# Kernel optimization log

Measured on AMD Instinct MI355X. Metric: run time of the kernel, lower is better.

## Reference

```python
import jax, jax.numpy as jnp
import numpy as np

B, N, C, H = 2, 1024, 1024, 16
HD = C // H
PAST = 8192
CACHE_BUDGET = 4000
ANCHOR = 512            # anchor_token_count (first-frame tokens preserved)
IMP_W = 0.5             # importance_weight
SCALE = HD ** -0.5


def setup_inputs() -> dict:
    key = jax.random.key(0)
    ks = jax.random.split(key, 8)
    return {
        "x": jax.random.normal(ks[0], (B, N, C), jnp.float32),
        "past_k": jax.random.normal(ks[1], (B, H, PAST, HD), jnp.float32),
        "past_v": jax.random.normal(ks[2], (B, H, PAST, HD), jnp.float32),
        "importance_scores": jax.random.uniform(ks[3], (B, N), dtype=jnp.float32),
        "qkv_w": jax.random.normal(ks[4], (3 * C, C), jnp.float32) * 0.02,
        "qkv_b": jnp.zeros((3 * C,), jnp.float32),
        "proj_w": jax.random.normal(ks[5], (C, C), jnp.float32) * 0.02,
        "proj_b": jnp.zeros((C,), jnp.float32),
    }


def _eviction(k, v, imp):
    # k, v: [B, H, Ntot, D]; imp: [B, N_new]. Hybrid branch of Attention.eviction.
    Bb, Hh, Ntot, D = k.shape
    A = ANCHOR
    Nc = Ntot - A                      # candidates
    keep = CACHE_BUDGET - A            # num_to_keep_from_candidates
    n_old = Nc - N                     # old (past-frame) candidates
    anchor_k, cand_k = k[:, :, :A], k[:, :, A:]
    anchor_v, cand_v = v[:, :, :A], v[:, :, A:]
    # cosine-diversity baseline (F.normalize uses eps=1e-12)
    kn = cand_k / jnp.maximum(jnp.linalg.norm(cand_k, axis=-1, keepdims=True), 1e-12)
    mean_vec = kn.mean(axis=2, keepdims=True)              # [B,H,1,D]
    baseline = jnp.sum(kn * mean_vec, axis=-1)             # [B,H,Nc]
    div_avg = (1.0 - baseline).mean(axis=1)                # [B,Nc]
    old = div_avg[:, :n_old]
    old_n = (old - old.min(axis=-1, keepdims=True)) / (
        old.max(axis=-1, keepdims=True) - old.min(axis=-1, keepdims=True) + 1e-8)
    new_n = (imp - imp.min(axis=-1, keepdims=True)) / (
        imp.max(axis=-1, keepdims=True) - imp.min(axis=-1, keepdims=True) + 1e-8)
    combined = jnp.concatenate([(1.0 - IMP_W) * old_n, IMP_W * new_n], axis=-1)  # [B,Nc]
    _, idx = jax.lax.top_k(combined, keep)
    idx = jnp.sort(idx, axis=-1)                           # [B,keep]
    gidx = jnp.broadcast_to(idx[:, None, :, None], (Bb, Hh, keep, D))
    kept_k = jnp.take_along_axis(cand_k, gidx, axis=2)
    kept_v = jnp.take_along_axis(cand_v, gidx, axis=2)
    return (jnp.concatenate([anchor_k, kept_k], axis=2),
            jnp.concatenate([anchor_v, kept_v], axis=2))


def reference(x, past_k, past_v, importance_scores, qkv_w, qkv_b, proj_w, proj_b):
    # qkv projection -> [3, B, H, N, HD]
    qkv = (x @ qkv_w.T + qkv_b).reshape(B, N, 3, H, HD).transpose(2, 0, 3, 1, 4)
    q, k, v = qkv[0], qkv[1], qkv[2]
    # append to KV cache
    k = jnp.concatenate([past_k, k], axis=2)
    v = jnp.concatenate([past_v, v], axis=2)
    # KV-cache eviction (topk importance + cosine diversity + gather compaction)
    k, v = _eviction(k, v, importance_scores)              # [B,H,CACHE_BUDGET,HD]
    # scaled dot-product attention
    attn = jax.nn.softmax(jnp.einsum('bhqd,bhkd->bhqk', q, k) * SCALE, axis=-1)
    out = jnp.einsum('bhqk,bhkd->bhqd', attn, v)
    out = out.transpose(0, 2, 1, 3).reshape(B, N, C)
    return out @ proj_w.T + proj_b
```

## Files before the change

kernel.cpp:

```cpp
#include <hip/hip_runtime.h>
#include <hip/hip_bf16.h>

typedef unsigned short u16;
typedef unsigned int   u32;
typedef __attribute__((ext_vector_type(8)))  short v8s;
typedef __attribute__((ext_vector_type(4)))  float v4f;
typedef __attribute__((ext_vector_type(16))) float v16f;
typedef __attribute__((ext_vector_type(4)))  u32   v4u;
typedef __attribute__((ext_vector_type(2)))  u32   v2u;

#define B_      2
#define N_      1024
#define C_      1024
#define H_      16
#define BH_     32
#define PAST_   8192
#define BUDGET  4000
#define ANCHOR_ 512
#define NCAND   8704
#define NOLD    7680
#define KEEPN   3488
#define NSPLIT  4
#define QSCALE  0.18033688011112042f

__device__ __forceinline__ u16 f2bf(float f) {
    u32 u = __float_as_uint(f);
    u32 r = u + 0x7fffu + ((u >> 16) & 1u);
    return (u16)(r >> 16);
}
__device__ __forceinline__ float bf2f(u16 h) {
    return __uint_as_float(((u32)h) << 16);
}
__device__ __forceinline__ u32 pk2(float a, float b) {
    __hip_bfloat162 t = __float22bfloat162_rn(float2{a, b});
    u32 r; __builtin_memcpy(&r, &t, 4); return r;
}
__device__ __forceinline__ v8s mk8(u32 a, u32 b, u32 c, u32 d) {
    union { u32 u[4]; v8s s; } t; t.u[0]=a; t.u[1]=b; t.u[2]=c; t.u[3]=d; return t.s;
}

__global__ void prep(const float* __restrict__ x, const float* __restrict__ qw,
                     const float* __restrict__ pw, u16* __restrict__ xcat,
                     u16* __restrict__ wcat, u16* __restrict__ wpbf) {
    const int i = blockIdx.x * 256 + threadIdx.x;
    const int NX = 2048 * 1024, NW = 3072 * 1024;
    if (i < NX) {
        float v = x[i];
        u16 hi = f2bf(v); float lo = v - bf2f(hi);
        const int m = i >> 10, k = i & 1023;
        u16* p = xcat + (size_t)m * 3072 + k;
        p[0] = hi; p[1024] = hi; p[2048] = f2bf(lo);
    } else if (i < NX + NW) {
        const int j = i - NX;
        float v = qw[j];
        u16 hi = f2bf(v); float lo = v - bf2f(hi);
        const int n = j >> 10, k = j & 1023;
        u16* p = wcat + (size_t)n * 3072 + k;
        p[0] = hi; p[1024] = f2bf(lo); p[2048] = hi;
    } else {
        const int j = i - NX - NW;
        wpbf[j] = f2bf(pw[j]);
    }
}

__global__ __launch_bounds__(256) void gemm_qkv(
    const u16* __restrict__ A, const u16* __restrict__ Bm,
    const float* __restrict__ bias,
    u16* __restrict__ Qbf, float* __restrict__ Vnew, float* __restrict__ Kpart) {
    __shared__ u16 As[128 * 72];
    __shared__ u16 Bs[128 * 72];
    const int tid = threadIdx.x;
    const int l = tid & 63, w = tid >> 6;
    const int wm = w >> 1, wn = w & 1;
    const int bid = blockIdx.x;
    int tsel, by, bx, s;
    if (bid < 128)      { tsel = 0; by = bid >> 3; bx = bid & 7; s = 0; }
    else if (bid < 256) { int r = bid - 128; tsel = 2; by = r >> 3; bx = r & 7; s = 0; }
    else                { int r = bid - 256; s = r >> 7; r &= 127; tsel = 1; by = r >> 3; bx = r & 7; }
    const int ks = s * 1024;
    const int nbase = tsel * 1024 + bx * 128;

    v4f acc[4][4];
    #pragma unroll
    for (int a = 0; a < 4; ++a)
        #pragma unroll
        for (int b = 0; b < 4; ++b) { acc[a][b][0]=0.f; acc[a][b][1]=0.f; acc[a][b][2]=0.f; acc[a][b][3]=0.f; }

    const int srow = tid >> 1, shalf = tid & 1;
    const u16* pa = A  + ((size_t)(by * 128 + srow)) * 3072 + ks + shalf * 32;
    const u16* pb = Bm + ((size_t)(nbase + srow))    * 3072 + ks + shalf * 32;
    v4u ar[4], br[4];
    #pragma unroll
    for (int j = 0; j < 4; ++j) { ar[j] = *(const v4u*)(pa + j * 8); br[j] = *(const v4u*)(pb + j * 8); }

    for (int k0 = 0; k0 < 1024; k0 += 64) {
        #pragma unroll
        for (int j = 0; j < 4; ++j) {
            *(v4u*)(&As[srow * 72 + shalf * 32 + j * 8]) = ar[j];
            *(v4u*)(&Bs[srow * 72 + shalf * 32 + j * 8]) = br[j];
        }
        __syncthreads();
        if (k0 + 64 < 1024) {
            #pragma unroll
            for (int j = 0; j < 4; ++j) {
                ar[j] = *(const v4u*)(pa + (k0 + 64) + j * 8);
                br[j] = *(const v4u*)(pb + (k0 + 64) + j * 8);
            }
        }
        #pragma unroll
        for (int kc = 0; kc < 2; ++kc) {
            v8s af[4], bfr[4];
            #pragma unroll
            for (int mt = 0; mt < 4; ++mt)
                af[mt] = *(const v8s*)(&As[(wm * 64 + mt * 16 + (l & 15)) * 72 + kc * 32 + (l >> 4) * 8]);
            #pragma unroll
            for (int nt = 0; nt < 4; ++nt)
                bfr[nt] = *(const v8s*)(&Bs[(wn * 64 + nt * 16 + (l & 15)) * 72 + kc * 32 + (l >> 4) * 8]);
            #pragma unroll
            for (int mt = 0; mt < 4; ++mt)
                #pragma unroll
                for (int nt = 0; nt < 4; ++nt)
                    acc[mt][nt] = __builtin_amdgcn_mfma_f32_16x16x32_bf16(af[mt], bfr[nt], acc[mt][nt], 0, 0, 0);
        }
        __syncthreads();
    }
    #pragma unroll
    for (int nt = 0; nt < 4; ++nt) {
        const int nl = bx * 128 + wn * 64 + nt * 16 + (l & 15);
        const int hh = nl >> 6, dd = nl & 63;
        const float bv = bias[tsel * 1024 + nl];
        #pragma unroll
        for (int mt = 0; mt < 4; ++mt)
            #pragma unroll
            for (int r = 0; r < 4; ++r) {
                const int m = by * 128 + wm * 64 + mt * 16 + (l >> 4) * 4 + r;
                const int bb = m >> 10, nn = m & 1023;
                const size_t o = (((size_t)(bb * 16 + hh)) * 1024 + nn) * 64 + dd;
                if (tsel == 0)      Qbf[o] = f2bf((acc[mt][nt][r] + bv) * QSCALE);
                else if (tsel == 2) Vnew[o] = acc[mt][nt][r] + bv;
                else                Kpart[(size_t)s * 2097152 + o] = acc[mt][nt][r] + (s == 0 ? bv : 0.f);
            }
    }
}

__global__ void kred(float* __restrict__ Kp) {
    const size_t i = ((size_t)blockIdx.x * 256 + threadIdx.x) * 4;
    v4f a = *(const v4f*)(Kp + i);
    v4f b = *(const v4f*)(Kp + 2097152 + i);
    v4f c = *(const v4f*)(Kp + 4194304 + i);
    #pragma unroll
    for (int e = 0; e < 4; ++e) a[e] = (a[e] + b[e]) + c[e];
    *(v4f*)(Kp + i) = a;
}

__global__ __launch_bounds__(256) void kmean(const float* __restrict__ past_k,
                                             const float* __restrict__ Knew,
                                             float* __restrict__ part) {
    __shared__ float Asum[4][64];
    const int blk = blockIdx.x, tid = threadIdx.x;
    const int bh = blk / 34, seg = blk % 34;
    const int l = tid & 63, w = tid >> 6;
    const int rr = l >> 4, dd = l & 15;
    v4f acc; acc[0]=0.f; acc[1]=0.f; acc[2]=0.f; acc[3]=0.f;
    const int base = seg * 256 + w * 64;
    for (int q4 = 0; q4 < 64; q4 += 4) {
        const int i = base + q4 + rr;
        const float* rp = (i < NOLD)
            ? past_k + (((size_t)bh * PAST_) + ANCHOR_ + i) * 64
            : Knew   + (((size_t)bh * N_) + (i - NOLD)) * 64;
        v4f v = *(const v4f*)(rp + dd * 4);
        float ss = v[0]*v[0] + v[1]*v[1] + v[2]*v[2] + v[3]*v[3];
        ss += __shfl_xor(ss, 1); ss += __shfl_xor(ss, 2);
        ss += __shfl_xor(ss, 4); ss += __shfl_xor(ss, 8);
        const float rn = 1.0f / fmaxf(sqrtf(ss), 1e-12f);
        acc[0] += v[0]*rn; acc[1] += v[1]*rn; acc[2] += v[2]*rn; acc[3] += v[3]*rn;
    }
    #pragma unroll
    for (int e = 0; e < 4; ++e) { acc[e] += __shfl_xor(acc[e], 16); acc[e] += __shfl_xor(acc[e], 32); }
    if (l < 16) *(v4f*)(&Asum[w][dd * 4]) = acc;
    __syncthreads();
    if (tid < 64) {
        float s = Asum[0][tid] + Asum[1][tid] + Asum[2][tid] + Asum[3][tid];
        part[((size_t)seg * BH_ + bh) * 64 + tid] = s;
    }
}

__global__ void kmr(const float* __restrict__ part, float* __restrict__ msum) {
    const int i = blockIdx.x * 256 + threadIdx.x;
    if (i < 2048) {
        float s = 0.f;
        for (int g = 0; g < 34; ++g) s += part[(size_t)g * 2048 + i];
        msum[i] = s;
    }
}

__global__ __launch_bounds__(256) void kdiv(const float* __restrict__ past_k,
                                            const float* __restrict__ msum,
                                            float* __restrict__ divavg) {
    __shared__ float MV[1024];
    const int blk = blockIdx.x, tid = threadIdx.x;
    const int b = blk / 240, ib = blk % 240;
    for (int j = tid; j < 1024; j += 256) MV[j] = msum[(size_t)b * 1024 + j] / 8704.0f;
    __syncthreads();
    const int l = tid & 63, w = tid >> 6;
    const int rr = l >> 4, dd = l & 15;
    for (int ii = 0; ii < 8; ++ii) {
        const int i = ib * 32 + w * 8 + ii;
        float accv = 0.f;
        #pragma unroll
        for (int hq = 0; hq < 4; ++hq) {
            const int h = hq * 4 + rr;
            const v4f v  = *(const v4f*)(past_k + (((size_t)(b * 16 + h)) * PAST_ + ANCHOR_ + i) * 64 + dd * 4);
            const v4f mv = *(const v4f*)(&MV[h * 64 + dd * 4]);
            float ss = v[0]*v[0] + v[1]*v[1] + v[2]*v[2] + v[3]*v[3];
            float dp = v[0]*mv[0] + v[1]*mv[1] + v[2]*mv[2] + v[3]*mv[3];
            ss += __shfl_xor(ss, 1); dp += __shfl_xor(dp, 1);
            ss += __shfl_xor(ss, 2); dp += __shfl_xor(dp, 2);
            ss += __shfl_xor(ss, 4); dp += __shfl_xor(dp, 4);
            ss += __shfl_xor(ss, 8); dp += __shfl_xor(dp, 8);
            accv += 1.0f - dp / fmaxf(sqrtf(ss), 1e-12f);
        }
        accv += __shfl_xor(accv, 16); accv += __shfl_xor(accv, 32);
        if (l == 0) divavg[(size_t)b * NOLD + i] = accv / 16.0f;
    }
}

__global__ __launch_bounds__(256) void kselect(const float* __restrict__ divavg,
                                               const float* __restrict__ imp,
                                               int* __restrict__ keep) {
    __shared__ float comb[NCAND];
    __shared__ float red[16];
    __shared__ u32 scnt[2][4];
    __shared__ u32 sg[257], se[257];
    const int b = blockIdx.x, tid = threadIdx.x;
    const int l = tid & 63, w = tid >> 6;

    float mn = 1e30f, mx = -1e30f;
    for (int i = tid; i < NOLD; i += 256) { float v = divavg[b * NOLD + i]; mn = fminf(mn, v); mx = fmaxf(mx, v); }
    #pragma unroll
    for (int d = 1; d < 64; d <<= 1) { mn = fminf(mn, __shfl_xor(mn, d)); mx = fmaxf(mx, __shfl_xor(mx, d)); }
    if (l == 0) { red[w] = mn; red[4 + w] = mx; }
    float mn2 = 1e30f, mx2 = -1e30f;
    for (int i = tid; i < N_; i += 256) { float v = imp[b * N_ + i]; mn2 = fminf(mn2, v); mx2 = fmaxf(mx2, v); }
    #pragma unroll
    for (int d = 1; d < 64; d <<= 1) { mn2 = fminf(mn2, __shfl_xor(mn2, d)); mx2 = fmaxf(mx2, __shfl_xor(mx2, d)); }
    if (l == 0) { red[8 + w] = mn2; red[12 + w] = mx2; }
    __syncthreads();
    const float omin = fminf(fminf(red[0], red[1]), fminf(red[2], red[3]));
    const float omax = fmaxf(fmaxf(red[4], red[5]), fmaxf(red[6], red[7]));
    const float imin = fminf(fminf(red[8], red[9]), fminf(red[10], red[11]));
    const float imax = fmaxf(fmaxf(red[12], red[13]), fmaxf(red[14], red[15]));
    const float oden = omax - omin + 1e-8f, iden = imax - imin + 1e-8f;
    for (int i = tid; i < NCAND; i += 256)
        comb[i] = (i < NOLD) ? 0.5f * ((divavg[b * NOLD + i] - omin) / oden)
                             : 0.5f * ((imp[b * N_ + i - NOLD] - imin) / iden);
    __syncthreads();
    u32 fu[34];
    const int i0 = tid * 34;
    #pragma unroll
    for (int j = 0; j < 34; ++j) fu[j] = __float_as_uint(comb[i0 + j]);
    u32 lo = 0, hi = 0x3F000000u;
    int it = 0;
    while (lo < hi) {
        const u32 mid = lo + ((hi - lo) >> 1);
        u32 c = 0;
        #pragma unroll
        for (int j = 0; j < 34; ++j) c += (fu[j] > mid) ? 1u : 0u;
        c += __shfl_xor(c, 1); c += __shfl_xor(c, 2); c += __shfl_xor(c, 4);
        c += __shfl_xor(c, 8); c += __shfl_xor(c, 16); c += __shfl_xor(c, 32);
        if (l == 0) scnt[it & 1][w] = c;
        __syncthreads();
        const u32 total = scnt[it & 1][0] + scnt[it & 1][1] + scnt[it & 1][2] + scnt[it & 1][3];
        if (total < KEEPN) hi = mid; else lo = mid + 1;
        ++it;
    }
    const u32 tau = lo;
    u32 ng = 0, ne = 0;
    #pragma unroll
    for (int j = 0; j < 34; ++j) { ng += (fu[j] > tau); ne += (fu[j] == tau); }
    sg[tid + 1] = ng; se[tid + 1] = ne;
    __syncthreads();
    if (tid == 0) { sg[0] = 0; se[0] = 0; for (int t = 1; t <= 256; ++t) { sg[t] += sg[t - 1]; se[t] += se[t - 1]; } }
    __syncthreads();
    const u32 need = KEEPN - sg[256];
    u32 g = sg[tid], e = se[tid];
    #pragma unroll
    for (int j = 0; j < 34; ++j) {
        const u32 u = fu[j];
        const bool kg = u > tau;
        const bool ke = (u == tau) && (e < need);
        if (kg || ke) keep[b * KEEPN + (g + (e < need ? e : need))] = 512 + i0 + j;
        g += kg ? 1u : 0u; e += (u == tau) ? 1u : 0u;
    }
}

__global__ __launch_bounds__(256) void kgather(const float* __restrict__ past_k,
    const float* __restrict__ past_v, const float* __restrict__ Knew,
    const float* __restrict__ Vnew, const int* __restrict__ keep,
    u16* __restrict__ Kg, u16* __restrict__ VTg) {
    __shared__ float VL[64][65];
    const int blk = blockIdx.x, tid = threadIdx.x;
    const int bh = blk / 63, jb = blk % 63;
    const int b = bh >> 4;
    const int jj = tid >> 2, cc = tid & 3;
    const int j = jb * 64 + jj;
    if (j < BUDGET) {
        const int row = (j < ANCHOR_) ? j : keep[b * KEEPN + (j - ANCHOR_)];
        const float *ks, *vs;
        if (row < PAST_) { size_t o = ((size_t)bh * PAST_ + row) * 64; ks = past_k + o; vs = past_v + o; }
        else             { size_t o = ((size_t)bh * N_ + (row - PAST_)) * 64; ks = Knew + o; vs = Vnew + o; }
        union { u16 h[16]; v4u v[2]; } pk_;
        #pragma unroll
        for (int q4 = 0; q4 < 4; ++q4) {
            v4f kv = *(const v4f*)(ks + cc * 16 + q4 * 4);
            v4f vv = *(const v4f*)(vs + cc * 16 + q4 * 4);
            #pragma unroll
            for (int e = 0; e < 4; ++e) {
                pk_.h[q4 * 4 + e] = f2bf(kv[e]);
                VL[jj][cc * 16 + q4 * 4 + e] = vv[e];
            }
        }
        v4u* kout = (v4u*)(Kg + ((size_t)bh * BUDGET + j) * 64 + cc * 16);
        kout[0] = pk_.v[0]; kout[1] = pk_.v[1];
    }
    __syncthreads();
    const int d = tid >> 2, c4 = tid & 3;
    const int jc = c4 * 16;
    if (jb * 64 + jc < BUDGET) {
        union { u16 h[16]; v4u v[2]; } pv_;
        #pragma unroll
        for (int t2 = 0; t2 < 16; ++t2) pv_.h[t2] = f2bf(VL[jc + t2][d]);
        v4u* vout = (v4u*)(VTg + ((size_t)bh * 64 + d) * BUDGET + jb * 64 + jc);
        vout[0] = pv_.v[0]; vout[1] = pv_.v[1];
    }
}

__global__ __launch_bounds__(256) void attn(const u16* __restrict__ Qbf,
    const u16* __restrict__ Kg, const u16* __restrict__ VTg,
    float* __restrict__ Opart, float* __restrict__ Mpart, float* __restrict__ Lpart) {
    __shared__ u16 Ks[2][32 * 72];
    __shared__ u16 Vs[2][64 * 40];
    const int tid = threadIdx.x;
    const int l = tid & 63, w = tid >> 6;
    const int G = l >> 5, lq = l & 31;
    const int bid = blockIdx.x;
    const int bh = bid >> 5, rem = bid & 31;
    const int split = rem & 3, qblk = rem >> 2;
    const int q = qblk * 128 + w * 32 + lq;
    const int t0 = split * 32;
    const int t1 = (split == 3) ? 125 : (t0 + 32);

    v8s Qf[4];
    const v8s* qp = (const v8s*)(Qbf + ((size_t)(bh * 1024 + q)) * 64);
    #pragma unroll
    for (int c = 0; c < 4; ++c) Qf[c] = qp[c * 2 + G];

    v16f o0, o1;
    #pragma unroll
    for (int e = 0; e < 16; ++e) { o0[e] = 0.f; o1[e] = 0.f; }
    float mrun = -1e30f, lrun = 0.f;

    const int krow = tid >> 3, kc8 = tid & 7;
    const int vrow = tid >> 2, vc4 = tid & 3;
    const u16* kbase = Kg + ((size_t)bh * BUDGET + krow) * 64 + kc8 * 8;
    const u16* vbase = VTg + ((size_t)bh * 64 + vrow) * BUDGET + vc4 * 8;
    v4u kreg = *(const v4u*)(kbase + (size_t)t0 * 2048);
    v4u vreg = *(const v4u*)(vbase + t0 * 32);
    int cur = 0;

    for (int t = t0; t < t1; ++t) {
        *(v4u*)(&Ks[cur][krow * 72 + kc8 * 8]) = kreg;
        *(v4u*)(&Vs[cur][vrow * 40 + vc4 * 8]) = vreg;
        if (t + 1 < t1) {
            kreg = *(const v4u*)(kbase + (size_t)(t + 1) * 2048);
            vreg = *(const v4u*)(vbase + (t + 1) * 32);
        }
        __syncthreads();
        v16f s;
        #pragma unroll
        for (int e = 0; e < 16; ++e) s[e] = 0.f;
        v8s kf[4];
        #pragma unroll
        for (int c = 0; c < 4; ++c) kf[c] = *(const v8s*)(&Ks[cur][lq * 72 + c * 16 + G * 8]);
        #pragma unroll
        for (int c = 0; c < 4; ++c)
            s = __builtin_amdgcn_mfma_f32_32x32x16_bf16(kf[c], Qf[c], s, 0, 0, 0);
        float m0 = fmaxf(s[0], s[1]),  m1 = fmaxf(s[2], s[3]),  m2 = fmaxf(s[4], s[5]),  m3 = fmaxf(s[6], s[7]);
        float m4 = fmaxf(s[8], s[9]),  m5 = fmaxf(s[10], s[11]), m6 = fmaxf(s[12], s[13]), m7 = fmaxf(s[14], s[15]);
        float mt = fmaxf(fmaxf(fmaxf(m0, m1), fmaxf(m2, m3)), fmaxf(fmaxf(m4, m5), fmaxf(m6, m7)));
        mt = fmaxf(mt, __shfl_xor(mt, 32));
        if (__any(mt > mrun + 8.0f)) {
            const float mnew = fmaxf(mrun, mt);
            const float alpha = exp2f(mrun - mnew);
            #pragma unroll
            for (int e = 0; e < 16; ++e) { o0[e] *= alpha; o1[e] *= alpha; }
            lrun *= alpha;
            mrun = mnew;
        }
        float p[16];
        #pragma unroll
        for (int e = 0; e < 16; ++e) p[e] = exp2f(s[e] - mrun);
        float l0 = (p[0] + p[1]) + (p[2] + p[3]), l1 = (p[4] + p[5]) + (p[6] + p[7]);
        float l2 = (p[8] + p[9]) + (p[10] + p[11]), l3 = (p[12] + p[13]) + (p[14] + p[15]);
        lrun += (l0 + l1) + (l2 + l3);
        u32 dP[8];
        #pragma unroll
        for (int e = 0; e < 8; ++e) dP[e] = pk2(p[2 * e], p[2 * e + 1]);
        const u32 sA = G ? dP[0] : dP[2]; const u32 rA = __shfl_xor(sA, 32);
        const u32 sB = G ? dP[1] : dP[3]; const u32 rB = __shfl_xor(sB, 32);
        const u32 sC = G ? dP[4] : dP[6]; const u32 rC = __shfl_xor(sC, 32);
        const u32 sD = G ? dP[5] : dP[7]; const u32 rD = __shfl_xor(sD, 32);
        const v8s P0 = mk8(G ? rA : dP[0], G ? rB : dP[1], G ? dP[2] : rA, G ? dP[3] : rB);
        const v8s P1 = mk8(G ? rC : dP[4], G ? rD : dP[5], G ? dP[6] : rC, G ? dP[7] : rD);
        #pragma unroll
        for (int kc = 0; kc < 2; ++kc) {
            const v8s Pf = kc ? P1 : P0;
            v8s va = *(const v8s*)(&Vs[cur][lq * 40 + kc * 16 + G * 8]);
            v8s vb = *(const v8s*)(&Vs[cur][(32 + lq) * 40 + kc * 16 + G * 8]);
            o0 = __builtin_amdgcn_mfma_f32_32x32x16_bf16(va, Pf, o0, 0, 0, 0);
            o1 = __builtin_amdgcn_mfma_f32_32x32x16_bf16(vb, Pf, o1, 0, 0, 0);
        }
        cur ^= 1;
    }
    const float ltot = lrun + __shfl_xor(lrun, 32);
    const size_t base = (((size_t)(split * 32 + bh)) * 1024 + q) * 64;
    #pragma unroll
    for (int c = 0; c < 2; ++c) {
        #pragma unroll
        for (int rq = 0; rq < 4; ++rq) {
            v4f v;
            #pragma unroll
            for (int e = 0; e < 4; ++e) v[e] = (c ? o1[4 * rq + e] : o0[4 * rq + e]);
            *(v4f*)(Opart + base + 32 * c + 8 * rq + 4 * G) = v;
        }
    }
    if (G == 0) {
        Mpart[(size_t)(split * 32 + bh) * 1024 + q] = mrun;
        Lpart[(size_t)(split * 32 + bh) * 1024 + q] = ltot;
    }
}

__global__ void kmerge(const float* __restrict__ Op, const float* __restrict__ Mp,
                       const float* __restrict__ Lp, u16* __restrict__ attnbf) {
    const int idx = blockIdx.x * 256 + threadIdx.x;
    const int dq = idx & 15, q = (idx >> 4) & 1023, bh = idx >> 14;
    float m[NSPLIT], li[NSPLIT];
    #pragma unroll
    for (int s = 0; s < NSPLIT; ++s) {
        m[s]  = Mp[(size_t)(s * 32 + bh) * 1024 + q];
        li[s] = Lp[(size_t)(s * 32 + bh) * 1024 + q];
    }
    const float M = fmaxf(fmaxf(m[0], m[1]), fmaxf(m[2], m[3]));
    float ww[NSPLIT]; float den = 0.f;
    #pragma unroll
    for (int s = 0; s < NSPLIT; ++s) { ww[s] = exp2f(m[s] - M); den += ww[s] * li[s]; }
    const float rden = 1.0f / den;
    v4f acc; acc[0]=0.f; acc[1]=0.f; acc[2]=0.f; acc[3]=0.f;
    #pragma unroll
    for (int s = 0; s < NSPLIT; ++s) {
        const v4f a = *(const v4f*)(Op + ((((size_t)(s * 32 + bh)) * 1024 + q) * 64) + dq * 4);
        #pragma unroll
        for (int e = 0; e < 4; ++e) acc[e] += ww[s] * a[e];
    }
    union { u16 h[4]; v2u v; } r_;
    #pragma unroll
    for (int e = 0; e < 4; ++e) r_.h[e] = f2bf(acc[e] * rden);
    const int bb = bh >> 4, h = bh & 15;
    *(v2u*)(attnbf + ((size_t)(bb * 1024 + q)) * 1024 + h * 64 + dq * 4) = r_.v;
}

__global__ __launch_bounds__(256) void gemm_proj64(
    const u16* __restrict__ A, const u16* __restrict__ Bm,
    const float* __restrict__ bias, float* __restrict__ Cout) {
    __shared__ u16 As[64 * 72];
    __shared__ u16 Bs[64 * 72];
    const int tid = threadIdx.x;
    const int l = tid & 63, w = tid >> 6;
    const int wm = w >> 1, wn = w & 1;
    const int by = blockIdx.x >> 4, bx = blockIdx.x & 15;
    v4f acc[2][2];
    #pragma unroll
    for (int a = 0; a < 2; ++a)
        #pragma unroll
        for (int b = 0; b < 2; ++b) { acc[a][b][0]=0.f; acc[a][b][1]=0.f; acc[a][b][2]=0.f; acc[a][b][3]=0.f; }

    const int srow = tid >> 2, sq = tid & 3;
    const u16* pa = A  + ((size_t)(by * 64 + srow)) * 1024 + sq * 16;
    const u16* pb = Bm + ((size_t)(bx * 64 + srow)) * 1024 + sq * 16;
    v4u ar[2], br[2];
    #pragma unroll
    for (int j = 0; j < 2; ++j) { ar[j] = *(const v4u*)(pa + j * 8); br[j] = *(const v4u*)(pb + j * 8); }

    for (int k0 = 0; k0 < 1024; k0 += 64) {
        #pragma unroll
        for (int j = 0; j < 2; ++j) {
            *(v4u*)(&As[srow * 72 + sq * 16 + j * 8]) = ar[j];
            *(v4u*)(&Bs[srow * 72 + sq * 16 + j * 8]) = br[j];
        }
        __syncthreads();
        if (k0 + 64 < 1024) {
            #pragma unroll
            for (int j = 0; j < 2; ++j) {
                ar[j] = *(const v4u*)(pa + (k0 + 64) + j * 8);
                br[j] = *(const v4u*)(pb + (k0 + 64) + j * 8);
            }
        }
        #pragma unroll
        for (int kc = 0; kc < 2; ++kc) {
            v8s af[2], bfr[2];
            #pragma unroll
            for (int mt = 0; mt < 2; ++mt)
                af[mt] = *(const v8s*)(&As[(wm * 32 + mt * 16 + (l & 15)) * 72 + kc * 32 + (l >> 4) * 8]);
            #pragma unroll
            for (int nt = 0; nt < 2; ++nt)
                bfr[nt] = *(const v8s*)(&Bs[(wn * 32 + nt * 16 + (l & 15)) * 72 + kc * 32 + (l >> 4) * 8]);
            #pragma unroll
            for (int mt = 0; mt < 2; ++mt)
                #pragma unroll
                for (int nt = 0; nt < 2; ++nt)
                    acc[mt][nt] = __builtin_amdgcn_mfma_f32_16x16x32_bf16(af[mt], bfr[nt], acc[mt][nt], 0, 0, 0);
        }
        __syncthreads();
    }
    #pragma unroll
    for (int nt = 0; nt < 2; ++nt) {
        const int n = bx * 64 + wn * 32 + nt * 16 + (l & 15);
        const float bv = bias[n];
        #pragma unroll
        for (int mt = 0; mt < 2; ++mt)
            #pragma unroll
            for (int r = 0; r < 4; ++r) {
                const int m = by * 64 + wm * 32 + mt * 16 + (l >> 4) * 4 + r;
                Cout[(size_t)m * 1024 + n] = acc[mt][nt][r] + bv;
            }
    }
}

extern "C" void kernel_launch(void* const* d_in, const int* in_sizes, int n_in,
                              void* d_out, int out_size, void* d_ws, size_t ws_size,
                              hipStream_t stream) {
    const float* x      = (const float*)d_in[0];
    const float* past_k = (const float*)d_in[1];
    const float* past_v = (const float*)d_in[2];
    const float* imp    = (const float*)d_in[3];
    const float* qkv_w  = (const float*)d_in[4];
    const float* qkv_b  = (const float*)d_in[5];
    const float* proj_w = (const float*)d_in[6];
    const float* proj_b = (const float*)d_in[7];
    float* out = (float*)d_out;
    char* ws = (char*)d_ws;

    const size_t o_kg    = 0;
    const size_t o_vtg   = 16384000;
    const size_t o_xcat  = 0;
    const size_t o_wcat  = 12582912;
    const size_t o_abf   = 0;
    const size_t o_wproj = 32768000;
    const size_t o_qbf   = 34865152;
    const size_t o_opart = 39059456;
    const size_t o_kpart = 39059456;
    const size_t o_vnew  = 64225280;
    const size_t o_part  = 72613888;
    const size_t o_msum  = 72892416;
    const size_t o_div   = 72900608;
    const size_t o_keep  = 72962048;
    const size_t o_mpart = 72989952;
    const size_t o_lpart = 73514240;
    const size_t total   = 74038528;
    if (ws_size < total) return;

    u16*   xcat  = (u16*)(ws + o_xcat);
    u16*   wcat  = (u16*)(ws + o_wcat);
    u16*   Kg    = (u16*)(ws + o_kg);
    u16*   VTg   = (u16*)(ws + o_vtg);
    u16*   wproj = (u16*)(ws + o_wproj);
    u16*   Qbf   = (u16*)(ws + o_qbf);
    float* Kpart = (float*)(ws + o_kpart);
    float* Knew  = Kpart;
    float* Vnew  = (float*)(ws + o_vnew);
    float* Opart = (float*)(ws + o_opart);
    float* part  = (float*)(ws + o_part);
    float* msum  = (float*)(ws + o_msum);
    float* divavg= (float*)(ws + o_div);
    int*   keep  = (int*)(ws + o_keep);
    float* Mpart = (float*)(ws + o_mpart);
    float* Lpart = (float*)(ws + o_lpart);
    u16*   attnbf= (u16*)(ws + o_abf);

    prep<<<24576, 256, 0, stream>>>(x, qkv_w, proj_w, xcat, wcat, wproj);
    gemm_qkv<<<640, 256, 0, stream>>>(xcat, wcat, qkv_b, Qbf, Vnew, Kpart);
    kred<<<2048, 256, 0, stream>>>(Kpart);
    kmean<<<1088, 256, 0, stream>>>(past_k, Knew, part);
    kmr<<<8, 256, 0, stream>>>(part, msum);
    kdiv<<<480, 256, 0, stream>>>(past_k, msum, divavg);
    kselect<<<2, 256, 0, stream>>>(divavg, imp, keep);
    kgather<<<2016, 256, 0, stream>>>(past_k, past_v, Knew, Vnew, keep, Kg, VTg);
    attn<<<1024, 256, 0, stream>>>(Qbf, Kg, VTg, Opart, Mpart, Lpart);
    kmerge<<<2048, 256, 0, stream>>>(Opart, Mpart, Lpart, attnbf);
    gemm_proj64<<<512, 256, 0, stream>>>(attnbf, wproj, proj_b, out);
}
```

Before: 248.9 us.

## Shrink attention blocks to two waves, swizzle block order, use permlane32_swap and setprio

The attention kernel now launches 2048 blocks of 128 threads, each covering 64 queries instead of 128, with launch bounds asking for 3 blocks per CU. Block indices are remapped so neighbouring blocks land on different XCD slices. The cross-half P-fragment exchange uses permlane32_swap instead of shfl_xor plus selects, and MFMA sections are wrapped in s_setprio. The smaller blocks aim for better occupancy and scheduling, but each K/V tile loaded into shared memory is now reused by half as many queries, doubling K/V traffic per query.

```diff
diff --git a/kernel.cpp b/kernel.cpp
--- a/kernel.cpp
+++ b/kernel.cpp
@@ -36,7 +36,8 @@
     u32 r; __builtin_memcpy(&r, &t, 4); return r;
 }
 __device__ __forceinline__ v8s mk8(u32 a, u32 b, u32 c, u32 d) {
-    union { u32 u[4]; v8s s; } t; t.u[0]=a; t.u[1]=b; t.u[2]=c; t.u[3]=d; return t.s;
+    v4u t; t[0] = a; t[1] = b; t[2] = c; t[3] = d;
+    return __builtin_bit_cast(v8s, t);
 }
 
 __global__ void prep(const float* __restrict__ x, const float* __restrict__ qw,
@@ -335,7 +336,7 @@
     }
 }
 
-__global__ __launch_bounds__(256) void attn(const u16* __restrict__ Qbf,
+__global__ __launch_bounds__(128, 3) void attn(const u16* __restrict__ Qbf,
     const u16* __restrict__ Kg, const u16* __restrict__ VTg,
     float* __restrict__ Opart, float* __restrict__ Mpart, float* __restrict__ Lpart) {
     __shared__ u16 Ks[2][32 * 72];
@@ -343,10 +344,10 @@
     const int tid = threadIdx.x;
     const int l = tid & 63, w = tid >> 6;
     const int G = l >> 5, lq = l & 31;
-    const int bid = blockIdx.x;
-    const int bh = bid >> 5, rem = bid & 31;
+    const int bid = ((blockIdx.x & 7) << 8) | (blockIdx.x >> 3);
+    const int bh = bid >> 6, rem = bid & 63;
     const int split = rem & 3, qblk = rem >> 2;
-    const int q = qblk * 128 + w * 32 + lq;
+    const int q = qblk * 64 + w * 32 + lq;
     const int t0 = split * 32;
     const int t1 = (split == 3) ? 125 : (t0 + 32);
 
@@ -360,20 +361,26 @@
     for (int e = 0; e < 16; ++e) { o0[e] = 0.f; o1[e] = 0.f; }
     float mrun = -1e30f, lrun = 0.f;
 
-    const int krow = tid >> 3, kc8 = tid & 7;
-    const int vrow = tid >> 2, vc4 = tid & 3;
-    const u16* kbase = Kg + ((size_t)bh * BUDGET + krow) * 64 + kc8 * 8;
-    const u16* vbase = VTg + ((size_t)bh * 64 + vrow) * BUDGET + vc4 * 8;
-    v4u kreg = *(const v4u*)(kbase + (size_t)t0 * 2048);
-    v4u vreg = *(const v4u*)(vbase + t0 * 32);
+    const int krow = tid >> 2, kc = tid & 3;
+    const int vrow = tid >> 1, vc = tid & 1;
+    const u16* kbase = Kg + ((size_t)bh * BUDGET + krow) * 64 + kc * 16;
+    const u16* vbase = VTg + ((size_t)bh * 64 + vrow) * BUDGET + vc * 16;
+    v4u kr0 = *(const v4u*)(kbase + (size_t)t0 * 2048);
+    v4u kr1 = *(const v4u*)(kbase + (size_t)t0 * 2048 + 8);
+    v4u vr0 = *(const v4u*)(vbase + t0 * 32);
+    v4u vr1 = *(const v4u*)(vbase + t0 * 32 + 8);
     int cur = 0;
 
     for (int t = t0; t < t1; ++t) {
-        *(v4u*)(&Ks[cur][krow * 72 + kc8 * 8]) = kreg;
-        *(v4u*)(&Vs[cur][vrow * 40 + vc4 * 8]) = vreg;
+        *(v4u*)(&Ks[cur][krow * 72 + kc * 16])     = kr0;
+        *(v4u*)(&Ks[cur][krow * 72 + kc * 16 + 8]) = kr1;
+        *(v4u*)(&Vs[cur][vrow * 40 + vc * 16])     = vr0;
+        *(v4u*)(&Vs[cur][vrow * 40 + vc * 16 + 8]) = vr1;
         if (t + 1 < t1) {
-            kreg = *(const v4u*)(kbase + (size_t)(t + 1) * 2048);
-            vreg = *(const v4u*)(vbase + (t + 1) * 32);
+            kr0 = *(const v4u*)(kbase + (size_t)(t + 1) * 2048);
+            kr1 = *(const v4u*)(kbase + (size_t)(t + 1) * 2048 + 8);
+            vr0 = *(const v4u*)(vbase + (t + 1) * 32);
+            vr1 = *(const v4u*)(vbase + (t + 1) * 32 + 8);
         }
         __syncthreads();
         v16f s;
@@ -382,9 +389,11 @@
         v8s kf[4];
         #pragma unroll
         for (int c = 0; c < 4; ++c) kf[c] = *(const v8s*)(&Ks[cur][lq * 72 + c * 16 + G * 8]);
+        __builtin_amdgcn_s_setprio(1);
         #pragma unroll
         for (int c = 0; c < 4; ++c)
             s = __builtin_amdgcn_mfma_f32_32x32x16_bf16(kf[c], Qf[c], s, 0, 0, 0);
+        __builtin_amdgcn_s_setprio(0);
         float m0 = fmaxf(s[0], s[1]),  m1 = fmaxf(s[2], s[3]),  m2 = fmaxf(s[4], s[5]),  m3 = fmaxf(s[6], s[7]);
         float m4 = fmaxf(s[8], s[9]),  m5 = fmaxf(s[10], s[11]), m6 = fmaxf(s[12], s[13]), m7 = fmaxf(s[14], s[15]);
         float mt = fmaxf(fmaxf(fmaxf(m0, m1), fmaxf(m2, m3)), fmaxf(fmaxf(m4, m5), fmaxf(m6, m7)));
@@ -406,20 +415,22 @@
         u32 dP[8];
         #pragma unroll
         for (int e = 0; e < 8; ++e) dP[e] = pk2(p[2 * e], p[2 * e + 1]);
-        const u32 sA = G ? dP[0] : dP[2]; const u32 rA = __shfl_xor(sA, 32);
-        const u32 sB = G ? dP[1] : dP[3]; const u32 rB = __shfl_xor(sB, 32);
-        const u32 sC = G ? dP[4] : dP[6]; const u32 rC = __shfl_xor(sC, 32);
-        const u32 sD = G ? dP[5] : dP[7]; const u32 rD = __shfl_xor(sD, 32);
-        const v8s P0 = mk8(G ? rA : dP[0], G ? rB : dP[1], G ? dP[2] : rA, G ? dP[3] : rB);
-        const v8s P1 = mk8(G ? rC : dP[4], G ? rD : dP[5], G ? dP[6] : rC, G ? dP[7] : rD);
-        #pragma unroll
-        for (int kc = 0; kc < 2; ++kc) {
-            const v8s Pf = kc ? P1 : P0;
-            v8s va = *(const v8s*)(&Vs[cur][lq * 40 + kc * 16 + G * 8]);
-            v8s vb = *(const v8s*)(&Vs[cur][(32 + lq) * 40 + kc * 16 + G * 8]);
-            o0 = __builtin_amdgcn_mfma_f32_32x32x16_bf16(va, Pf, o0, 0, 0, 0);
-            o1 = __builtin_amdgcn_mfma_f32_32x32x16_bf16(vb, Pf, o1, 0, 0, 0);
-        }
+        auto r02 = __builtin_amdgcn_permlane32_swap(dP[0], dP[2], false, false);
+        auto r13 = __builtin_amdgcn_permlane32_swap(dP[1], dP[3], false, false);
+        auto r46 = __builtin_amdgcn_permlane32_swap(dP[4], dP[6], false, false);
+        auto r57 = __builtin_amdgcn_permlane32_swap(dP[5], dP[7], false, false);
+        const v8s P0 = mk8(r02[0], r13[0], r02[1], r13[1]);
+        const v8s P1 = mk8(r46[0], r57[0], r46[1], r57[1]);
+        v8s va0 = *(const v8s*)(&Vs[cur][lq * 40 + G * 8]);
+        v8s vb0 = *(const v8s*)(&Vs[cur][(32 + lq) * 40 + G * 8]);
+        v8s va1 = *(const v8s*)(&Vs[cur][lq * 40 + 16 + G * 8]);
+        v8s vb1 = *(const v8s*)(&Vs[cur][(32 + lq) * 40 + 16 + G * 8]);
+        __builtin_amdgcn_s_setprio(1);
+        o0 = __builtin_amdgcn_mfma_f32_32x32x16_bf16(va0, P0, o0, 0, 0, 0);
+        o1 = __builtin_amdgcn_mfma_f32_32x32x16_bf16(vb0, P0, o1, 0, 0, 0);
+        o0 = __builtin_amdgcn_mfma_f32_32x32x16_bf16(va1, P1, o0, 0, 0, 0);
+        o1 = __builtin_amdgcn_mfma_f32_32x32x16_bf16(vb1, P1, o1, 0, 0, 0);
+        __builtin_amdgcn_s_setprio(0);
         cur ^= 1;
     }
     const float ltot = lrun + __shfl_xor(lrun, 32);
@@ -595,7 +606,7 @@
     kdiv<<<480, 256, 0, stream>>>(past_k, msum, divavg);
     kselect<<<2, 256, 0, stream>>>(divavg, imp, keep);
     kgather<<<2016, 256, 0, stream>>>(past_k, past_v, Knew, Vnew, keep, Kg, VTg);
-    attn<<<1024, 256, 0, stream>>>(Qbf, Kg, VTg, Opart, Mpart, Lpart);
+    attn<<<2048, 128, 0, stream>>>(Qbf, Kg, VTg, Opart, Mpart, Lpart);
     kmerge<<<2048, 256, 0, stream>>>(Opart, Mpart, Lpart, attnbf);
     gemm_proj64<<<512, 256, 0, stream>>>(attnbf, wproj, proj_b, out);
 }
```

Measured after the change: 240.5 us. 1.04x faster.
